# Kernel tuning notes

Hardware: AMD Instinct MI355X
Metric: run time of the kernel (lower is better)

## Reference

```python
import jax, jax.numpy as jnp
import numpy as np

EPS = 1e-8


def setup_inputs() -> dict:
    key = jax.random.key(0)
    k1, = jax.random.split(key, 1)
    # positive series (multiplicative Holt-Winters assumes positive data)
    x = jax.random.uniform(k1, (8192, 2048, 1), dtype=jnp.float32, minval=0.5, maxval=1.5)
    logit_alpha = jnp.zeros((), dtype=jnp.float32)
    logit_gamma = jnp.zeros((), dtype=jnp.float32)
    return {"x": x, "logit_alpha": logit_alpha, "logit_gamma": logit_gamma}


def reference(x, logit_alpha, logit_gamma):
    # x: (B, S, 1)
    alpha = jax.nn.sigmoid(logit_alpha)
    gamma = jax.nn.sigmoid(logit_gamma)

    l0 = x[:, 0, :]                      # (B, 1) initial level
    s0 = jnp.ones_like(l0)               # (B, 1) initial season
    y0 = x[:, 0, :] / (l0 * s0 + EPS)

    def step(carry, x_t):
        lp, sp = carry
        lt = alpha * (x_t / (sp + EPS)) + (1.0 - alpha) * lp
        st = gamma * (x_t / (lt + EPS)) + (1.0 - gamma) * sp
        yt = x_t / (lt * st + EPS)
        return (lt, st), (lt, st, yt)

    xs = jnp.swapaxes(x[:, 1:, :], 0, 1)  # (S-1, B, 1): scan over time
    _, (ls, ss, ys) = jax.lax.scan(step, (l0, s0), xs)

    def assemble(first, rest):
        # first: (B,1), rest: (S-1,B,1) -> (B,S,1)
        return jnp.swapaxes(jnp.concatenate([first[None], rest], axis=0), 0, 1)

    level = assemble(l0, ls)
    season = assemble(s0, ss)
    y = assemble(y0, ys)
    return level, season, y
```

## Files before the change

### kernel.cpp

```cpp
#include <hip/hip_runtime.h>
#include <math.h>


constexpr int   T    = 2048;
constexpr int   B    = 8192;
constexpr int   RPB  = 32;
constexpr int   TT   = 64;
constexpr int   NTI  = T / TT;
constexpr int   LSX  = 68;
constexpr float EPS  = 1e-8f;

__device__ __forceinline__ void lds_barrier() {
    __builtin_amdgcn_sched_barrier(0);
    asm volatile("s_waitcnt lgkmcnt(0)" ::: "memory");
    __builtin_amdgcn_s_barrier();
    __builtin_amdgcn_sched_barrier(0);
}

__global__ __launch_bounds__(192, 1)
void hw_kernel(const float* __restrict__ x,
               const float* __restrict__ pla,
               const float* __restrict__ plg,
               float* __restrict__ out)
{
    __shared__ alignas(16) float LT[2][RPB][LSX];
    __shared__ alignas(16) float DT[2][RPB][LSX];

    const int tid  = threadIdx.x;
    const int wid  = tid >> 6;
    const int lane = tid & 63;
    const int row0 = blockIdx.x * RPB;

    const float alpha = 1.0f / (1.0f + expf(-pla[0]));
    const float gamma = 1.0f / (1.0f + expf(-plg[0]));
    const float oma = 1.0f - alpha, omg = 1.0f - gamma;
    const float EPSa = EPS * alpha;
    const float EPSg = EPS * gamma;

    float* __restrict__ lout = out;
    float* __restrict__ sout = out + (size_t)B * T;
    float* __restrict__ yout = out + (size_t)2 * B * T;

    const int cr = lane >> 4;
    const int cc = (lane & 15) << 2;

    auto store_tile = [&](int m, int itlo, int ithi) {
        const int bsel = m & 1;
        const int t0 = m * TT;
        #pragma unroll
        for (int it = itlo; it < ithi; ++it) {
            const int r = 4 * it + cr;
            const size_t g = (size_t)(row0 + r) * T + t0 + cc;
            const float4 vl = *reinterpret_cast<const float4*>(&LT[bsel][r][cc]);
            const float4 vd = *reinterpret_cast<const float4*>(&DT[bsel][r][cc]);
            const float4 xv = *reinterpret_cast<const float4*>(&x[g]);
            float4 vs, vy;
            vs.x = vd.x * __builtin_amdgcn_rcpf(vl.x);
            vs.y = vd.y * __builtin_amdgcn_rcpf(vl.y);
            vs.z = vd.z * __builtin_amdgcn_rcpf(vl.z);
            vs.w = vd.w * __builtin_amdgcn_rcpf(vl.w);
            vy.x = xv.x * __builtin_amdgcn_rcpf(vd.x);
            vy.y = xv.y * __builtin_amdgcn_rcpf(vd.y);
            vy.z = xv.z * __builtin_amdgcn_rcpf(vd.z);
            vy.w = xv.w * __builtin_amdgcn_rcpf(vd.w);
            *reinterpret_cast<float4*>(&lout[g]) = vl;
            *reinterpret_cast<float4*>(&sout[g]) = vs;
            *reinterpret_cast<float4*>(&yout[g]) = vy;
        }
    };

    if (wid == 0) {
        const bool act = lane < RPB;
        const float* __restrict__ xrow = x + (size_t)(row0 + (act ? lane : 0)) * T;

        float lte = 0.0f;
        float D   = 1.0f;
        float v   = 1.0f;
        float4 XA[16], XB[16];

        auto loadX = [&](float4* Xb, int k) {
            const float* p = xrow + k * TT;
            #pragma unroll
            for (int i = 0; i < 16; ++i)
                Xb[i] = *reinterpret_cast<const float4*>(p + 4 * i);
        };

        auto do_step = [&](float xt, float& lo, float& dsto) {
            const float ax  = alpha * xt;
            const float gx  = gamma * xt;
            const float cl  = __builtin_fmaf(oma, lte, EPSa);
            const float pre = __builtin_fmaf(oma, D, ax);
            const float ltn = __builtin_fmaf(ax, v, cl);
            const float K   = __builtin_fmaf(EPSg, ltn, gx);
            const float Dn  = __builtin_fmaf(omg, pre, K);
            const float un  = __builtin_amdgcn_rcpf(Dn);
            const float vn  = ltn * un;
            lo = ltn; dsto = Dn;
            lte = ltn; D = Dn; v = vn;
        };

        auto compute_tile = [&](const float4* Xb, int k, bool first) {
            const int bsel = k & 1;
            #pragma unroll
            for (int g = 0; g < 16; ++g) {
                const float4 xv = Xb[g];
                float4 lv, dv;
                if (first && g == 0) {
                    lte = xv.x + EPS;
                    const float ste0 = 1.0f + EPS;
                    D = lte * ste0;
                    v = lte * __builtin_amdgcn_rcpf(D);
                    lv.x = lte; dv.x = D;
                    do_step(xv.y, lv.y, dv.y);
                    do_step(xv.z, lv.z, dv.z);
                    do_step(xv.w, lv.w, dv.w);
                } else {
                    do_step(xv.x, lv.x, dv.x);
                    do_step(xv.y, lv.y, dv.y);
                    do_step(xv.z, lv.z, dv.z);
                    do_step(xv.w, lv.w, dv.w);
                }
                *reinterpret_cast<float4*>(&LT[bsel][lane][4 * g]) = lv;
                *reinterpret_cast<float4*>(&DT[bsel][lane][4 * g]) = dv;
            }
        };

        if (act) { loadX(XA, 0); loadX(XB, 1); }
        if (act) compute_tile(XA, 0, true);
        lds_barrier();

        #pragma unroll 1
        for (int k = 1; k < NTI - 1; k += 2) {
            if (act) { loadX(XA, k + 1); compute_tile(XB, k, false); }
            lds_barrier();
            if (act) { loadX(XB, k + 2); compute_tile(XA, k + 1, false); }
            lds_barrier();
        }
        if (act) compute_tile(XB, NTI - 1, false);
        lds_barrier();
    } else {
        const int lo = (wid - 1) * 4;
        #pragma unroll 1
        for (int k = 0; k < NTI; ++k) {
            if (k > 0) store_tile(k - 1, lo, lo + 4);
            lds_barrier();
        }
    }

    {
        const int lo = (wid == 0) ? 0 : (wid == 1) ? 2 : 5;
        const int hi = (wid == 0) ? 2 : (wid == 1) ? 5 : 8;
        store_tile(NTI - 1, lo, hi);
    }
}

extern "C" void kernel_launch(void* const* d_in, const int* in_sizes, int n_in,
                              void* d_out, int out_size, void* d_ws, size_t ws_size,
                              hipStream_t stream) {
    const float* x   = (const float*)d_in[0];
    const float* pla = (const float*)d_in[1];
    const float* plg = (const float*)d_in[2];
    float* out = (float*)d_out;

    dim3 grid(B / RPB);
    dim3 block(192);
    hw_kernel<<<grid, block, 0, stream>>>(x, pla, plg, out);
}
```

Measured before the change: 62.72 us.

## Move x loads and per-step scaling to store waves via LDS staging

The two store warps now load x for the next tile and precompute alpha*x and a combined coefficient c1*x into a double-buffered LDS array. The serial recurrence warp reads these from LDS instead of holding 32 float4 register buffers and issuing global loads. The recurrence is algebraically folded so each step has one fewer dependent FMA. This shortens the critical serial chain and cuts register pressure, but adds LDS traffic and reads x twice from global memory (preprocess and store). It also changes floating-point rounding slightly.

Result: slower. 67.48 us (+7.6%).

```diff
diff --git a/kernel.cpp b/kernel.cpp
--- a/kernel.cpp
+++ b/kernel.cpp
@@ -8,6 +8,7 @@
 constexpr int   TT   = 64;
 constexpr int   NTI  = T / TT;
 constexpr int   LSX  = 68;
+constexpr int   AWS  = 132;
 constexpr float EPS  = 1e-8f;
 
 __device__ __forceinline__ void lds_barrier() {
@@ -25,6 +26,7 @@
 {
     __shared__ alignas(16) float LT[2][RPB][LSX];
     __shared__ alignas(16) float DT[2][RPB][LSX];
+    __shared__ alignas(16) float AW[2][RPB][AWS];
 
     const int tid  = threadIdx.x;
     const int wid  = tid >> 6;
@@ -36,6 +38,8 @@
     const float oma = 1.0f - alpha, omg = 1.0f - gamma;
     const float EPSa = EPS * alpha;
     const float EPSg = EPS * gamma;
+    const float c1   = alpha + gamma - alpha * gamma;
+    const float c2   = oma * omg;
 
     float* __restrict__ lout = out;
     float* __restrict__ sout = out + (size_t)B * T;
@@ -69,80 +73,83 @@
         }
     };
 
+    auto preprocess = [&](int k, int itlo, int ithi) {
+        const int bsel = k & 1;
+        const int t0 = k * TT;
+        #pragma unroll
+        for (int it = itlo; it < ithi; ++it) {
+            const int r = 4 * it + cr;
+            const size_t g = (size_t)(row0 + r) * T + t0 + cc;
+            const float4 xv = *reinterpret_cast<const float4*>(&x[g]);
+            float4 p0, p1;
+            p0.x = alpha * xv.x; p0.y = c1 * xv.x;
+            p0.z = alpha * xv.y; p0.w = c1 * xv.y;
+            p1.x = alpha * xv.z; p1.y = c1 * xv.z;
+            p1.z = alpha * xv.w; p1.w = c1 * xv.w;
+            *reinterpret_cast<float4*>(&AW[bsel][r][2 * cc])     = p0;
+            *reinterpret_cast<float4*>(&AW[bsel][r][2 * cc + 4]) = p1;
+        }
+    };
+
     if (wid == 0) {
         const bool act = lane < RPB;
-        const float* __restrict__ xrow = x + (size_t)(row0 + (act ? lane : 0)) * T;
+        const float x0v = act ? x[(size_t)(row0 + lane) * T] : 1.0f;
 
         float lte = 0.0f;
         float D   = 1.0f;
         float v   = 1.0f;
-        float4 XA[16], XB[16];
 
-        auto loadX = [&](float4* Xb, int k) {
-            const float* p = xrow + k * TT;
-            #pragma unroll
-            for (int i = 0; i < 16; ++i)
-                Xb[i] = *reinterpret_cast<const float4*>(p + 4 * i);
-        };
-
-        auto do_step = [&](float xt, float& lo, float& dsto) {
-            const float ax  = alpha * xt;
-            const float gx  = gamma * xt;
+        auto do_step = [&](float ax, float W, float& lo, float& dsto) {
             const float cl  = __builtin_fmaf(oma, lte, EPSa);
-            const float pre = __builtin_fmaf(oma, D, ax);
+            const float cD  = __builtin_fmaf(c2, D, W);
             const float ltn = __builtin_fmaf(ax, v, cl);
-            const float K   = __builtin_fmaf(EPSg, ltn, gx);
-            const float Dn  = __builtin_fmaf(omg, pre, K);
+            const float Dn  = __builtin_fmaf(EPSg, ltn, cD);
             const float un  = __builtin_amdgcn_rcpf(Dn);
             const float vn  = ltn * un;
             lo = ltn; dsto = Dn;
             lte = ltn; D = Dn; v = vn;
         };
 
-        auto compute_tile = [&](const float4* Xb, int k, bool first) {
+        auto compute_tile = [&](int k, bool first) {
             const int bsel = k & 1;
             #pragma unroll
             for (int g = 0; g < 16; ++g) {
-                const float4 xv = Xb[g];
+                const float4 r0 = *reinterpret_cast<const float4*>(&AW[bsel][lane][8 * g]);
+                const float4 r1 = *reinterpret_cast<const float4*>(&AW[bsel][lane][8 * g + 4]);
                 float4 lv, dv;
                 if (first && g == 0) {
-                    lte = xv.x + EPS;
-                    const float ste0 = 1.0f + EPS;
-                    D = lte * ste0;
-                    v = lte * __builtin_amdgcn_rcpf(D);
+                    lte = x0v + EPS;
+                    D   = lte * (1.0f + EPS);
+                    v   = lte * __builtin_amdgcn_rcpf(D);
                     lv.x = lte; dv.x = D;
-                    do_step(xv.y, lv.y, dv.y);
-                    do_step(xv.z, lv.z, dv.z);
-                    do_step(xv.w, lv.w, dv.w);
+                    do_step(r0.z, r0.w, lv.y, dv.y);
+                    do_step(r1.x, r1.y, lv.z, dv.z);
+                    do_step(r1.z, r1.w, lv.w, dv.w);
                 } else {
-                    do_step(xv.x, lv.x, dv.x);
-                    do_step(xv.y, lv.y, dv.y);
-                    do_step(xv.z, lv.z, dv.z);
-                    do_step(xv.w, lv.w, dv.w);
+                    do_step(r0.x, r0.y, lv.x, dv.x);
+                    do_step(r0.z, r0.w, lv.y, dv.y);
+                    do_step(r1.x, r1.y, lv.z, dv.z);
+                    do_step(r1.z, r1.w, lv.w, dv.w);
                 }
                 *reinterpret_cast<float4*>(&LT[bsel][lane][4 * g]) = lv;
                 *reinterpret_cast<float4*>(&DT[bsel][lane][4 * g]) = dv;
             }
         };
 
-        if (act) { loadX(XA, 0); loadX(XB, 1); }
-        if (act) compute_tile(XA, 0, true);
         lds_barrier();
-
         #pragma unroll 1
-        for (int k = 1; k < NTI - 1; k += 2) {
-            if (act) { loadX(XA, k + 1); compute_tile(XB, k, false); }
-            lds_barrier();
-            if (act) { loadX(XB, k + 2); compute_tile(XA, k + 1, false); }
+        for (int k = 0; k < NTI; ++k) {
+            if (act) compute_tile(k, k == 0);
             lds_barrier();
         }
-        if (act) compute_tile(XB, NTI - 1, false);
-        lds_barrier();
     } else {
         const int lo = (wid - 1) * 4;
+        preprocess(0, lo, lo + 4);
+        lds_barrier();
         #pragma unroll 1
         for (int k = 0; k < NTI; ++k) {
-            if (k > 0) store_tile(k - 1, lo, lo + 4);
+            if (k + 1 < NTI) preprocess(k + 1, lo, lo + 4);
+            if (k > 0)       store_tile(k - 1, lo, lo + 4);
             lds_barrier();
         }
     }
```
